# Kernel tuning notes

Hardware: AMD Instinct MI355X
Metric: run time of the kernel (lower is better)

Reference implementation:

```python
import math
import jax, jax.numpy as jnp
import numpy as np

B, T, C, H = 2, 1024, 1024, 16
D = C // H
NEG = -jnp.inf


def setup_inputs() -> dict:
    key = jax.random.key(0)
    ks = jax.random.split(key, 4)
    x_star = jax.random.normal(ks[0], (B, T, C), jnp.float32)
    x_hat = jax.random.normal(ks[1], (B, T, C), jnp.float32)
    # attn_masks semantics: True = keep. star-keys: causal; hat-keys: diagonal only.
    keep_star = jnp.broadcast_to(jnp.tril(jnp.ones((T, T), bool)), (B, T, T))
    keep_hat = jnp.broadcast_to(jnp.eye(T, dtype=bool), (B, T, T))
    W_attn = jax.random.normal(ks[2], (C, 3 * C), jnp.float32) * (1.0 / math.sqrt(C))
    b_attn = jnp.zeros((3 * C,), jnp.float32)
    W_proj = jax.random.normal(ks[3], (C, C), jnp.float32) * (1.0 / math.sqrt(C))
    b_proj = jnp.zeros((C,), jnp.float32)
    return dict(x_star=x_star, x_hat=x_hat, keep_star=keep_star, keep_hat=keep_hat,
                W_attn=W_attn, b_attn=b_attn, W_proj=W_proj, b_proj=b_proj)


def _interleave(x_star, x_hat, keep_star, keep_hat, W_attn, b_attn, W_proj, b_proj):
    def qkv(x):
        q, k, v = jnp.split(x @ W_attn + b_attn, 3, axis=-1)
        r = lambda t: t.reshape(B, T, H, D).transpose(0, 2, 1, 3)  # (B,H,T,D)
        return r(q), r(k), r(v)

    q_s, k_s, v_s = qkv(x_star)
    q_h, k_h, v_h = qkv(x_hat)

    scale = 1.0 / math.sqrt(D)
    attend = lambda q, k: jnp.einsum('bhqd,bhkd->bhqk', q, k) * scale

    # blocking masks (True = block), broadcast over heads
    mask_star = ~keep_star[:, None, :, :]
    mask_hat = ~keep_hat[:, None, :, :]
    mask_causal = ~jnp.tril(jnp.ones((T, T), bool))[None, None]

    def mlp(y):  # (B,H,T,D) -> (B,T,C)
        y = y.transpose(0, 2, 1, 3).reshape(B, T, C)
        return y @ W_proj + b_proj  # resid_dropout is identity in eval

    # star stream: plain causal self-attention
    att_star = jnp.where(mask_causal, NEG, attend(q_s, k_s))
    y_star = mlp(jax.nn.softmax(att_star, axis=-1) @ v_s)

    # hat stream: merge two score streams (hat queries vs star keys / hat keys)
    att_hs = jnp.where(mask_star, NEG, attend(q_h, k_s))
    att_hh = jnp.where(mask_hat, NEG, attend(q_h, k_h))
    merged = jnp.where(jnp.isinf(att_hh), att_hs, att_hh)
    p = jax.nn.softmax(merged, axis=-1)
    y_hat = (jnp.where(mask_star, 0.0, p) @ v_s
             + jnp.where(mask_hat, 0.0, p) @ v_h)
    y_hat = mlp(y_hat)
    return y_star, y_hat


def reference(x_star, x_hat, keep_star, keep_hat, W_attn, b_attn, W_proj, b_proj):
    return _interleave(x_star, x_hat, keep_star, keep_hat, W_attn, b_attn, W_proj, b_proj)
```

## Files before the change

kernel.cpp:

```cpp
#include <hip/hip_runtime.h>
#include <math.h>

#define T_ 1024
#define C_ 1024
#define H_ 16
#define D_ 64
#define B_ 2
#define M2 (B_*T_*C_)
#define QSC 0.18033688f

typedef __attribute__((ext_vector_type(8))) short bf16x8;
typedef __attribute__((ext_vector_type(8))) unsigned short ushort8;
typedef __attribute__((ext_vector_type(4))) float f32x4;

__device__ inline float fast_exp2(float x) {
  return __builtin_amdgcn_exp2f(x);
}

__device__ inline unsigned short f2bf(float f) {
  unsigned int u = __float_as_uint(f);
  u += 0x7fff + ((u >> 16) & 1);
  return (unsigned short)(u >> 16);
}
__device__ inline float bf2f(unsigned short u) {
  return __uint_as_float(((unsigned int)u) << 16);
}
__device__ inline unsigned int pack2bf(float lo, float hi) {
  unsigned int ul = __float_as_uint(lo);
  unsigned int uh = __float_as_uint(hi);
  ul += 0x7fff + ((ul >> 16) & 1);
  uh += 0x7fff + ((uh >> 16) & 1);
  return (ul >> 16) | (uh & 0xffff0000u);
}

__device__ inline void load16(unsigned short* lds, const unsigned short* g) {
  __builtin_amdgcn_global_load_lds(
      (const __attribute__((address_space(1))) unsigned int*)g,
      (__attribute__((address_space(3))) unsigned int*)lds, 16, 0, 0);
}

__device__ void transpose_tile(const float* __restrict__ Win,
                               unsigned short* __restrict__ Wout, int N,
                               int n0, int k0, float (*Ts)[65], int tid)
{
#pragma unroll
  for (int p = 0; p < 4; ++p) {
    int chunk = tid + p * 256;
    int r = chunk >> 4, c4 = chunk & 15;
    float4 v = *(const float4*)(Win + (size_t)(k0 + r) * N + n0 + c4 * 4);
    Ts[r][c4*4+0] = v.x; Ts[r][c4*4+1] = v.y;
    Ts[r][c4*4+2] = v.z; Ts[r][c4*4+3] = v.w;
  }
  __syncthreads();
#pragma unroll
  for (int p = 0; p < 2; ++p) {
    int chunk = tid + p * 256;
    int n = chunk >> 3, kq = chunk & 7;
    ushort8 o;
#pragma unroll
    for (int j = 0; j < 8; ++j) o[j] = f2bf(Ts[kq * 8 + j][n]);
    *(ushort8*)(Wout + (size_t)(n0 + n) * 1024 + k0 + kq * 8) = o;
  }
}

__global__ __launch_bounds__(256) void prepass(
    const float* __restrict__ xs, const float* __restrict__ xh,
    const float* __restrict__ Wa, const float* __restrict__ Wp,
    unsigned short* __restrict__ Xbf, unsigned short* __restrict__ WaT,
    unsigned short* __restrict__ WpT)
{
  __shared__ float Ts[64][65];
  const int bid = blockIdx.x;
  const int tid = threadIdx.x;
  if (bid < 4096) {
    size_t c = (size_t)bid * 256 + tid;
    size_t e = c * 4;
    const float* src = (e < (size_t)2048 * 1024) ? (xs + e)
                                                 : (xh + e - (size_t)2048 * 1024);
    float4 v = *(const float4*)src;
    ushort4 o;
    o.x = f2bf(v.x); o.y = f2bf(v.y); o.z = f2bf(v.z); o.w = f2bf(v.w);
    *(ushort4*)(Xbf + e) = o;
  } else if (bid < 4864) {
    int t = bid - 4096;
    transpose_tile(Wa, WaT, 3072, (t % 48) * 64, (t / 48) * 64, Ts, tid);
  } else {
    int t = bid - 4864;
    transpose_tile(Wp, WpT, 1024, (t % 16) * 64, (t / 16) * 64, Ts, tid);
  }
}

__global__ __launch_bounds__(512) void qkv_mfma(
    const unsigned short* __restrict__ A,
    const unsigned short* __restrict__ Bt,
    const float* __restrict__ bias,
    unsigned short* __restrict__ qkv)
{
  __shared__ __align__(16) unsigned short As[128 * 64];
  __shared__ __align__(16) unsigned short Bs[128 * 64];
  const int tid = threadIdx.x;
  const int col0 = blockIdx.x * 128;
  const int row0 = blockIdx.y * 128;
  const int w = tid >> 6, lane = tid & 63;
  const int lane16 = lane & 15, quad = lane >> 4;
  const int wm = w >> 2, wn = w & 3;
  f32x4 acc[4][2];
#pragma unroll
  for (int mt = 0; mt < 4; ++mt)
#pragma unroll
    for (int nt = 0; nt < 2; ++nt) acc[mt][nt] = (f32x4){0.f, 0.f, 0.f, 0.f};

  for (int k0 = 0; k0 < 1024; k0 += 64) {
    __syncthreads();
#pragma unroll
    for (int it = 0; it < 2; ++it) {
      int chunk = tid + it * 512;
      int row = chunk >> 3, cq = chunk & 7, gq = cq ^ (row & 7);
      load16(As + chunk * 8, A  + (size_t)(row0 + row) * 1024 + k0 + gq * 8);
      load16(Bs + chunk * 8, Bt + (size_t)(col0 + row) * 1024 + k0 + gq * 8);
    }
    __syncthreads();
#pragma unroll
    for (int kb = 0; kb < 2; ++kb) {
      bf16x8 af[4], bfr[2];
      int q = kb * 4 + quad;
#pragma unroll
      for (int mt = 0; mt < 4; ++mt) {
        int m = wm * 64 + mt * 16 + lane16;
        af[mt] = *(const bf16x8*)&As[m * 64 + (q ^ (m & 7)) * 8];
      }
#pragma unroll
      for (int nt = 0; nt < 2; ++nt) {
        int n = wn * 32 + nt * 16 + lane16;
        bfr[nt] = *(const bf16x8*)&Bs[n * 64 + (q ^ (n & 7)) * 8];
      }
#pragma unroll
      for (int mt = 0; mt < 4; ++mt)
#pragma unroll
        for (int nt = 0; nt < 2; ++nt)
          acc[mt][nt] = __builtin_amdgcn_mfma_f32_16x16x32_bf16(
              af[mt], bfr[nt], acc[mt][nt], 0, 0, 0);
    }
  }

#pragma unroll
  for (int mt = 0; mt < 4; ++mt) {
#pragma unroll
    for (int nt = 0; nt < 2; ++nt) {
      int gn = col0 + wn * 32 + nt * 16 + lane16;
      int which = gn >> 10, c = gn & 1023;
      int h = c >> 6, d = c & 63;
      float bv = bias[gn];
#pragma unroll
      for (int r = 0; r < 4; ++r) {
        int gm = row0 + wm * 64 + mt * 16 + quad * 4 + r;
        int s = gm >> 11, b = (gm >> 10) & 1, t = gm & 1023;
        float val = acc[mt][nt][r] + bv;
        if (which == 0) val *= QSC;
        size_t idx;
        if (which == 2 && s == 0)
          idx = (size_t)2 * M2 + ((size_t)(b * 16 + h) * 64 + d) * 1024 + t;
        else
          idx = (size_t)(s * 3 + which) * M2 +
                ((size_t)(b * 16 + h) * 1024 + t) * 64 + d;
        qkv[idx] = f2bf(val);
      }
    }
  }
}

__global__ __launch_bounds__(256) void proj_mfma(
    const unsigned short* __restrict__ A,
    const unsigned short* __restrict__ Bt,
    const float* __restrict__ bias,
    float* __restrict__ out)
{
  __shared__ __align__(16) unsigned short As[128 * 64];
  __shared__ __align__(16) unsigned short Bs[64 * 64];
  const int tid = threadIdx.x;
  const int col0 = blockIdx.x * 64;
  const int row0 = blockIdx.y * 128;
  const int w = tid >> 6, lane = tid & 63;
  const int lane16 = lane & 15, quad = lane >> 4;
  const int wm = w >> 1, wn = w & 1;
  f32x4 acc[4][2];
#pragma unroll
  for (int mt = 0; mt < 4; ++mt)
#pragma unroll
    for (int nt = 0; nt < 2; ++nt) acc[mt][nt] = (f32x4){0.f, 0.f, 0.f, 0.f};

  for (int k0 = 0; k0 < 1024; k0 += 64) {
    __syncthreads();
#pragma unroll
    for (int it = 0; it < 4; ++it) {
      int chunk = tid + it * 256;
      int row = chunk >> 3, cq = chunk & 7, gq = cq ^ (row & 7);
      load16(As + chunk * 8, A + (size_t)(row0 + row) * 1024 + k0 + gq * 8);
    }
#pragma unroll
    for (int it = 0; it < 2; ++it) {
      int chunk = tid + it * 256;
      int row = chunk >> 3, cq = chunk & 7, gq = cq ^ (row & 7);
      load16(Bs + chunk * 8, Bt + (size_t)(col0 + row) * 1024 + k0 + gq * 8);
    }
    __syncthreads();
#pragma unroll
    for (int kb = 0; kb < 2; ++kb) {
      bf16x8 af[4], bfr[2];
      int q = kb * 4 + quad;
#pragma unroll
      for (int mt = 0; mt < 4; ++mt) {
        int m = wm * 64 + mt * 16 + lane16;
        af[mt] = *(const bf16x8*)&As[m * 64 + (q ^ (m & 7)) * 8];
      }
#pragma unroll
      for (int nt = 0; nt < 2; ++nt) {
        int n = wn * 32 + nt * 16 + lane16;
        bfr[nt] = *(const bf16x8*)&Bs[n * 64 + (q ^ (n & 7)) * 8];
      }
#pragma unroll
      for (int mt = 0; mt < 4; ++mt)
#pragma unroll
        for (int nt = 0; nt < 2; ++nt)
          acc[mt][nt] = __builtin_amdgcn_mfma_f32_16x16x32_bf16(
              af[mt], bfr[nt], acc[mt][nt], 0, 0, 0);
    }
  }

#pragma unroll
  for (int mt = 0; mt < 4; ++mt) {
#pragma unroll
    for (int nt = 0; nt < 2; ++nt) {
      int gn = col0 + wn * 32 + nt * 16 + lane16;
      float bv = bias[gn];
#pragma unroll
      for (int r = 0; r < 4; ++r) {
        int gm = row0 + wm * 64 + mt * 16 + quad * 4 + r;
        out[(size_t)gm * 1024 + gn] = acc[mt][nt][r] + bv;
      }
    }
  }
}

__global__ __launch_bounds__(256) void attn_fused(
    const unsigned short* __restrict__ ws, unsigned short* __restrict__ Y)
{
  __shared__ __align__(16) unsigned short Qss[64 * 64];
  __shared__ __align__(16) unsigned short Qsh[64 * 64];
  __shared__ __align__(16) unsigned short Ks[2][64 * 64];
  __shared__ __align__(16) unsigned short Vts[2][64 * 64];
  __shared__ __align__(16) unsigned short Ps[4][2][16][72];
  __shared__ float diag[64];

  const int tid = threadIdx.x;
  const int bx  = blockIdx.x;
  const int inner = bx & 31;
  const int h = inner & 15;
  const int b = (inner >> 4) & 1;
  const int qt = 15 - (bx >> 5);
  const int i0 = qt * 64;
  const size_t hb = (size_t)(b * H_ + h) * T_ * D_;

  const unsigned short* Qsg = ws + (size_t)0 * M2 + hb;
  const unsigned short* Kg  = ws + (size_t)1 * M2 + hb;
  const unsigned short* VTg = ws + (size_t)2 * M2 + hb;
  const unsigned short* Qhg = ws + (size_t)3 * M2 + hb;
  const unsigned short* Khg = ws + (size_t)4 * M2 + hb;
  const unsigned short* Vhg = ws + (size_t)5 * M2 + hb;

  const int lane = tid & 63;
  const int w = tid >> 6;
  const int lane16 = lane & 15, quad = lane >> 4;
  const int wq0 = w * 16;

#pragma unroll
  for (int it = 0; it < 2; ++it) {
    int ch = tid + it * 256;
    int row = ch >> 3, cq = ch & 7, gq = cq ^ (row & 7);
    load16(Qss + ch * 8, Qsg + (size_t)(i0 + row) * 64 + gq * 8);
    load16(Qsh + ch * 8, Qhg + (size_t)(i0 + row) * 64 + gq * 8);
    load16(&Ks[0][ch * 8], Kg + (size_t)row * 64 + gq * 8);
    load16(&Vts[0][ch * 8], VTg + (size_t)row * 1024 + gq * 8);
  }
  __syncthreads();

  bf16x8 qf[2][2];
  {
    int m = wq0 + lane16;
    qf[0][0] = *(const bf16x8*)&Qss[m * 64 + ((quad) ^ (m & 7)) * 8];
    qf[0][1] = *(const bf16x8*)&Qss[m * 64 + ((4 + quad) ^ (m & 7)) * 8];
    qf[1][0] = *(const bf16x8*)&Qsh[m * 64 + ((quad) ^ (m & 7)) * 8];
    qf[1][1] = *(const bf16x8*)&Qsh[m * 64 + ((4 + quad) ^ (m & 7)) * 8];
  }
  if (tid < 64) {
    const unsigned short* kh = Khg + (size_t)(i0 + tid) * 64;
    float sum = 0.f;
#pragma unroll
    for (int c = 0; c < 8; ++c) {
      bf16x8 qv = *(const bf16x8*)&Qsh[tid * 64 + (c ^ (tid & 7)) * 8];
      ushort8 kv = *(const ushort8*)(kh + c * 8);
#pragma unroll
      for (int j = 0; j < 8; ++j)
        sum += bf2f((unsigned short)qv[j]) * bf2f(kv[j]);
    }
    diag[tid] = sum;
  }
  __syncthreads();

  float lacc[2] = {0.f, 0.f};
  f32x4 O[2][4];
#pragma unroll
  for (int st = 0; st < 2; ++st)
#pragma unroll
    for (int nt = 0; nt < 4; ++nt) O[st][nt] = (f32x4){0.f, 0.f, 0.f, 0.f};
  const int kstar = wq0 + lane16;

  for (int kt = 0; kt <= qt; ++kt) {
    const int cur = kt & 1;
    if (kt < qt) {
      const int nxt = 1 - cur;
#pragma unroll
      for (int it = 0; it < 2; ++it) {
        int ch = tid + it * 256;
        int row = ch >> 3, cq = ch & 7, gq = cq ^ (row & 7);
        load16(&Ks[nxt][ch * 8], Kg + (size_t)((kt + 1) * 64 + row) * 64 + gq * 8);
        load16(&Vts[nxt][ch * 8], VTg + (size_t)row * 1024 + (kt + 1) * 64 + gq * 8);
      }
    }

    bf16x8 kf[2][4], vf[2][4];
#pragma unroll
    for (int kb = 0; kb < 2; ++kb) {
      int q = kb * 4 + quad;
#pragma unroll
      for (int mt = 0; mt < 4; ++mt) {
        int m = mt * 16 + lane16;
        kf[kb][mt] = *(const bf16x8*)&Ks[cur][m * 64 + (q ^ (m & 7)) * 8];
        vf[kb][mt] = *(const bf16x8*)&Vts[cur][m * 64 + (q ^ (m & 7)) * 8];
      }
    }

    f32x4 St[2][4];
#pragma unroll
    for (int st = 0; st < 2; ++st)
#pragma unroll
      for (int mt = 0; mt < 4; ++mt) St[st][mt] = (f32x4){0.f, 0.f, 0.f, 0.f};
#pragma unroll
    for (int kb = 0; kb < 2; ++kb)
#pragma unroll
      for (int st = 0; st < 2; ++st)
#pragma unroll
        for (int mt = 0; mt < 4; ++mt)
          St[st][mt] = __builtin_amdgcn_mfma_f32_16x16x32_bf16(
              kf[kb][mt], qf[st][kb], St[st][mt], 0, 0, 0);

    if (kt == qt) {
      const float dv = diag[kstar];
#pragma unroll
      for (int mt = 0; mt < 4; ++mt)
#pragma unroll
        for (int r = 0; r < 4; ++r) {
          int key = mt * 16 + quad * 4 + r;
          if (key > kstar) { St[0][mt][r] = -INFINITY; St[1][mt][r] = -INFINITY; }
          if (key == kstar) St[1][mt][r] = dv;
        }
    }

#pragma unroll
    for (int st = 0; st < 2; ++st) {
      float rsum = 0.f;
#pragma unroll
      for (int mt = 0; mt < 4; ++mt)
#pragma unroll
        for (int r = 0; r < 4; ++r) {
          float p = fast_exp2(St[st][mt][r]);
          St[st][mt][r] = p;
          rsum += p;
        }
      lacc[st] += rsum;
    }

#pragma unroll
    for (int st = 0; st < 2; ++st)
#pragma unroll
      for (int mt = 0; mt < 4; ++mt) {
        *(unsigned int*)&Ps[w][st][lane16][mt * 16 + quad * 4] =
            pack2bf(St[st][mt][0], St[st][mt][1]);
        *(unsigned int*)&Ps[w][st][lane16][mt * 16 + quad * 4 + 2] =
            pack2bf(St[st][mt][2], St[st][mt][3]);
      }

#pragma unroll
    for (int kb = 0; kb < 2; ++kb) {
      bf16x8 pa[2];
#pragma unroll
      for (int st = 0; st < 2; ++st)
        pa[st] = *(const bf16x8*)&Ps[w][st][lane16][kb * 32 + quad * 8];
#pragma unroll
      for (int st = 0; st < 2; ++st)
#pragma unroll
        for (int nt = 0; nt < 4; ++nt)
          O[st][nt] = __builtin_amdgcn_mfma_f32_16x16x32_bf16(
              pa[st], vf[kb][nt], O[st][nt], 0, 0, 0);
    }

    if (kt == qt) {
      float pd = fast_exp2(diag[kstar]);
      float p4[4];
#pragma unroll
      for (int r = 0; r < 4; ++r) p4[r] = __shfl(pd, quad * 4 + r, 16);
#pragma unroll
      for (int r = 0; r < 4; ++r) {
        const unsigned short* vh = Vhg + (size_t)(i0 + wq0 + quad * 4 + r) * 64;
#pragma unroll
        for (int nt = 0; nt < 4; ++nt)
          O[1][nt][r] += p4[r] * bf2f(vh[nt * 16 + lane16]);
      }
    }
    __syncthreads();
  }

#pragma unroll
  for (int st = 0; st < 2; ++st) {
    lacc[st] += __shfl_xor(lacc[st], 16, 64);
    lacc[st] += __shfl_xor(lacc[st], 32, 64);
  }
  float l4[2][4];
#pragma unroll
  for (int st = 0; st < 2; ++st)
#pragma unroll
    for (int r = 0; r < 4; ++r)
      l4[st][r] = __shfl(lacc[st], quad * 4 + r, 16);
#pragma unroll
  for (int r = 0; r < 4; ++r) {
    int gi = i0 + wq0 + quad * 4 + r;
    float invs = 1.f / l4[0][r];
    float invh = 1.f / l4[1][r];
    unsigned short* ys = Y + ((size_t)(b * 1024 + gi)) * 1024 + h * 64;
    unsigned short* yh = Y + ((size_t)(2048 + b * 1024 + gi)) * 1024 + h * 64;
#pragma unroll
    for (int nt = 0; nt < 4; ++nt) {
      ys[nt * 16 + lane16] = f2bf(O[0][nt][r] * invs);
      yh[nt * 16 + lane16] = f2bf(O[1][nt][r] * invh);
    }
  }
}

extern "C" void kernel_launch(void* const* d_in, const int* in_sizes, int n_in,
                              void* d_out, int out_size, void* d_ws, size_t ws_size,
                              hipStream_t stream) {
  (void)in_sizes; (void)n_in; (void)out_size; (void)ws_size;
  const float* xs = (const float*)d_in[0];
  const float* xh = (const float*)d_in[1];
  const float* Wa = (const float*)d_in[4];
  const float* ba = (const float*)d_in[5];
  const float* Wp = (const float*)d_in[6];
  const float* bp = (const float*)d_in[7];

  unsigned short* qkv = (unsigned short*)d_ws;
  unsigned short* Ybf = qkv + (size_t)6 * M2;
  unsigned short* Xbf = Ybf + (size_t)4 * 1024 * 1024;
  unsigned short* WaT = Xbf + (size_t)4 * 1024 * 1024;
  unsigned short* WpT = WaT + (size_t)3 * 1024 * 1024;
  float* out = (float*)d_out;

  prepass   <<<5120, 256, 0, stream>>>(xs, xh, Wa, Wp, Xbf, WaT, WpT);
  qkv_mfma  <<<dim3(24, 32), 512, 0, stream>>>(Xbf, WaT, ba, qkv);
  attn_fused<<<dim3(512), 256, 0, stream>>>(qkv, Ybf);
  proj_mfma <<<dim3(16, 32), 256, 0, stream>>>(Ybf, WpT, bp, out);
}
```

Measured before the change: 181.5 us.

## Fuse all four stages into one persistent cooperative kernel with grid syncs

Replaces the four separate launches (prepass, QKV GEMM, attention, projection) with a single cooperative kernel of 512 blocks that runs each stage in turn, separated by grid-wide barriers. The QKV GEMM is retiled to 128x192 tiles so that 512 blocks cover it, and the attention and projection stages reuse the shared-memory buffer. The aim is to remove kernel launch gaps and tail effects between stages. In exchange, each stage is limited to 512 blocks at two blocks per CU, grid.sync adds its own cost, and the larger QKV tile may raise register pressure. If the cooperative launch fails, the code falls back to the original four kernels.

```diff
diff --git a/kernel.cpp b/kernel.cpp
--- a/kernel.cpp
+++ b/kernel.cpp
@@ -1,5 +1,8 @@
 #include <hip/hip_runtime.h>
+#include <hip/hip_cooperative_groups.h>
 #include <math.h>
+
+namespace cg = cooperative_groups;
 
 #define T_ 1024
 #define C_ 1024
@@ -8,6 +11,7 @@
 #define B_ 2
 #define M2 (B_*T_*C_)
 #define QSC 0.18033688f
+#define LDSZ 51456
 
 typedef __attribute__((ext_vector_type(8))) short bf16x8;
 typedef __attribute__((ext_vector_type(8))) unsigned short ushort8;
@@ -16,7 +20,6 @@
 __device__ inline float fast_exp2(float x) {
   return __builtin_amdgcn_exp2f(x);
 }
-
 __device__ inline unsigned short f2bf(float f) {
   unsigned int u = __float_as_uint(f);
   u += 0x7fff + ((u >> 16) & 1);
@@ -32,16 +35,15 @@
   uh += 0x7fff + ((uh >> 16) & 1);
   return (ul >> 16) | (uh & 0xffff0000u);
 }
-
 __device__ inline void load16(unsigned short* lds, const unsigned short* g) {
   __builtin_amdgcn_global_load_lds(
       (const __attribute__((address_space(1))) unsigned int*)g,
       (__attribute__((address_space(3))) unsigned int*)lds, 16, 0, 0);
 }
 
-__device__ void transpose_tile(const float* __restrict__ Win,
-                               unsigned short* __restrict__ Wout, int N,
-                               int n0, int k0, float (*Ts)[65], int tid)
+__device__ inline void transpose_tile(const float* __restrict__ Win,
+                                      unsigned short* __restrict__ Wout, int N,
+                                      int n0, int k0, float (*Ts)[65], int tid)
 {
 #pragma unroll
   for (int p = 0; p < 4; ++p) {
@@ -60,6 +62,393 @@
 #pragma unroll
     for (int j = 0; j < 8; ++j) o[j] = f2bf(Ts[kq * 8 + j][n]);
     *(ushort8*)(Wout + (size_t)(n0 + n) * 1024 + k0 + kq * 8) = o;
+  }
+  __syncthreads();
+}
+
+__global__ __launch_bounds__(256, 2) void mega(
+    const float* __restrict__ xs, const float* __restrict__ xh,
+    const float* __restrict__ Wa, const float* __restrict__ ba,
+    const float* __restrict__ Wp, const float* __restrict__ bp,
+    unsigned short* __restrict__ qkv, unsigned short* __restrict__ Ybf,
+    unsigned short* __restrict__ Xbf, unsigned short* __restrict__ WaT,
+    unsigned short* __restrict__ WpT, float* __restrict__ out)
+{
+  extern __shared__ __align__(16) char smem[];
+  cg::grid_group grid = cg::this_grid();
+  const int tid = threadIdx.x;
+  const int bx  = blockIdx.x;
+
+  {
+    float (*Ts)[65] = (float (*)[65])smem;
+#pragma unroll 1
+    for (int u = bx; u < 5120; u += 512) {
+      if (u < 4096) {
+        size_t c = (size_t)u * 256 + tid;
+        size_t e = c * 4;
+        const float* src = (e < (size_t)2048 * 1024)
+                               ? (xs + e) : (xh + e - (size_t)2048 * 1024);
+        float4 v = *(const float4*)src;
+        ushort4 o;
+        o.x = f2bf(v.x); o.y = f2bf(v.y); o.z = f2bf(v.z); o.w = f2bf(v.w);
+        *(ushort4*)(Xbf + e) = o;
+      } else if (u < 4864) {
+        int t = u - 4096;
+        transpose_tile(Wa, WaT, 3072, (t % 48) * 64, (t / 48) * 64, Ts, tid);
+      } else {
+        int t = u - 4864;
+        transpose_tile(Wp, WpT, 1024, (t % 16) * 64, (t / 16) * 64, Ts, tid);
+      }
+    }
+  }
+  grid.sync();
+
+  {
+    unsigned short* As = (unsigned short*)smem;
+    unsigned short* Bs = (unsigned short*)(smem + 16384);
+    const int w = tid >> 6, lane = tid & 63;
+    const int lane16 = lane & 15, quad = lane >> 4;
+    const int wm = w >> 1, wn = w & 1;
+    const int col0 = (bx & 15) * 192;
+    const int row0 = (bx >> 4) * 128;
+    f32x4 acc[4][6];
+#pragma unroll
+    for (int mt = 0; mt < 4; ++mt)
+#pragma unroll
+      for (int nt = 0; nt < 6; ++nt) acc[mt][nt] = (f32x4){0.f, 0.f, 0.f, 0.f};
+
+    for (int k0 = 0; k0 < 1024; k0 += 64) {
+      __syncthreads();
+#pragma unroll
+      for (int it = 0; it < 4; ++it) {
+        int ch = tid + it * 256;
+        int row = ch >> 3, cq = ch & 7, gq = cq ^ (row & 7);
+        load16(As + ch * 8, Xbf + (size_t)(row0 + row) * 1024 + k0 + gq * 8);
+      }
+#pragma unroll
+      for (int it = 0; it < 6; ++it) {
+        int ch = tid + it * 256;
+        int row = ch >> 3, cq = ch & 7, gq = cq ^ (row & 7);
+        load16(Bs + ch * 8, WaT + (size_t)(col0 + row) * 1024 + k0 + gq * 8);
+      }
+      __syncthreads();
+#pragma unroll
+      for (int kb = 0; kb < 2; ++kb) {
+        bf16x8 af[4], bfr[6];
+        int q = kb * 4 + quad;
+#pragma unroll
+        for (int mt = 0; mt < 4; ++mt) {
+          int m = wm * 64 + mt * 16 + lane16;
+          af[mt] = *(const bf16x8*)&As[m * 64 + (q ^ (m & 7)) * 8];
+        }
+#pragma unroll
+        for (int nt = 0; nt < 6; ++nt) {
+          int n = wn * 96 + nt * 16 + lane16;
+          bfr[nt] = *(const bf16x8*)&Bs[n * 64 + (q ^ (n & 7)) * 8];
+        }
+#pragma unroll
+        for (int mt = 0; mt < 4; ++mt)
+#pragma unroll
+          for (int nt = 0; nt < 6; ++nt)
+            acc[mt][nt] = __builtin_amdgcn_mfma_f32_16x16x32_bf16(
+                af[mt], bfr[nt], acc[mt][nt], 0, 0, 0);
+      }
+    }
+#pragma unroll
+    for (int mt = 0; mt < 4; ++mt) {
+#pragma unroll
+      for (int nt = 0; nt < 6; ++nt) {
+        int gn = col0 + wn * 96 + nt * 16 + lane16;
+        int which = gn >> 10, c2 = gn & 1023;
+        int hh = c2 >> 6, dd = c2 & 63;
+        float bv = ba[gn];
+#pragma unroll
+        for (int r = 0; r < 4; ++r) {
+          int gm = row0 + wm * 64 + mt * 16 + quad * 4 + r;
+          int ss = gm >> 11, bb = (gm >> 10) & 1, t = gm & 1023;
+          float val = acc[mt][nt][r] + bv;
+          if (which == 0) val *= QSC;
+          size_t idx;
+          if (which == 2 && ss == 0)
+            idx = (size_t)2 * M2 + ((size_t)(bb * 16 + hh) * 64 + dd) * 1024 + t;
+          else
+            idx = (size_t)(ss * 3 + which) * M2 +
+                  ((size_t)(bb * 16 + hh) * 1024 + t) * 64 + dd;
+          qkv[idx] = f2bf(val);
+        }
+      }
+    }
+  }
+  grid.sync();
+
+  {
+    unsigned short* Ks0 = (unsigned short*)smem;
+    unsigned short* Ks1 = (unsigned short*)(smem + 8192);
+    unsigned short* Vt0 = (unsigned short*)(smem + 16384);
+    unsigned short* Vt1 = (unsigned short*)(smem + 24576);
+    unsigned short* PsB = (unsigned short*)(smem + 32768);
+    float* diag = (float*)(smem + 51200);
+
+    const int inner = bx & 31;
+    const int h = inner & 15;
+    const int b = (inner >> 4) & 1;
+    const int g = bx >> 5;
+    const int qt = (bx < 256) ? (15 - g) : (g - 8);
+    const int i0 = qt * 64;
+    const size_t hb = (size_t)(b * H_ + h) * T_ * D_;
+
+    const unsigned short* Qsg = qkv + (size_t)0 * M2 + hb;
+    const unsigned short* Kg  = qkv + (size_t)1 * M2 + hb;
+    const unsigned short* VTg = qkv + (size_t)2 * M2 + hb;
+    const unsigned short* Qhg = qkv + (size_t)3 * M2 + hb;
+    const unsigned short* Khg = qkv + (size_t)4 * M2 + hb;
+    const unsigned short* Vhg = qkv + (size_t)5 * M2 + hb;
+
+    const int lane = tid & 63;
+    const int w = tid >> 6;
+    const int lane16 = lane & 15, quad = lane >> 4;
+    const int wq0 = w * 16;
+
+    bf16x8 qf[2][2];
+    {
+      const unsigned short* qs = Qsg + (size_t)(i0 + wq0 + lane16) * 64;
+      const unsigned short* qh = Qhg + (size_t)(i0 + wq0 + lane16) * 64;
+      qf[0][0] = *(const bf16x8*)(qs + quad * 8);
+      qf[0][1] = *(const bf16x8*)(qs + 32 + quad * 8);
+      qf[1][0] = *(const bf16x8*)(qh + quad * 8);
+      qf[1][1] = *(const bf16x8*)(qh + 32 + quad * 8);
+    }
+    if (tid < 64) {
+      const unsigned short* qh = Qhg + (size_t)(i0 + tid) * 64;
+      const unsigned short* kh = Khg + (size_t)(i0 + tid) * 64;
+      float sum = 0.f;
+#pragma unroll
+      for (int c2 = 0; c2 < 8; ++c2) {
+        ushort8 qv = *(const ushort8*)(qh + c2 * 8);
+        ushort8 kv = *(const ushort8*)(kh + c2 * 8);
+#pragma unroll
+        for (int j = 0; j < 8; ++j) sum += bf2f(qv[j]) * bf2f(kv[j]);
+      }
+      diag[tid] = sum;
+    }
+#pragma unroll
+    for (int it = 0; it < 2; ++it) {
+      int ch = tid + it * 256;
+      int row = ch >> 3, cq = ch & 7, gq = cq ^ (row & 7);
+      load16(Ks0 + ch * 8, Kg + (size_t)row * 64 + gq * 8);
+      load16(Vt0 + ch * 8, VTg + (size_t)row * 1024 + gq * 8);
+    }
+    __syncthreads();
+
+    float lacc[2] = {0.f, 0.f};
+    f32x4 O[2][4];
+#pragma unroll
+    for (int st = 0; st < 2; ++st)
+#pragma unroll
+      for (int nt = 0; nt < 4; ++nt) O[st][nt] = (f32x4){0.f, 0.f, 0.f, 0.f};
+    const int kstar = wq0 + lane16;
+
+    for (int kt = 0; kt <= qt; ++kt) {
+      unsigned short* KsCur = (kt & 1) ? Ks1 : Ks0;
+      unsigned short* VtCur = (kt & 1) ? Vt1 : Vt0;
+      if (kt < qt) {
+        unsigned short* KsNxt = (kt & 1) ? Ks0 : Ks1;
+        unsigned short* VtNxt = (kt & 1) ? Vt0 : Vt1;
+#pragma unroll
+        for (int it = 0; it < 2; ++it) {
+          int ch = tid + it * 256;
+          int row = ch >> 3, cq = ch & 7, gq = cq ^ (row & 7);
+          load16(KsNxt + ch * 8, Kg + (size_t)((kt + 1) * 64 + row) * 64 + gq * 8);
+          load16(VtNxt + ch * 8, VTg + (size_t)row * 1024 + (kt + 1) * 64 + gq * 8);
+        }
+      }
+
+      bf16x8 kf[2][4], vf[2][4];
+#pragma unroll
+      for (int kb = 0; kb < 2; ++kb) {
+        int q = kb * 4 + quad;
+#pragma unroll
+        for (int mt = 0; mt < 4; ++mt) {
+          int m = mt * 16 + lane16;
+          kf[kb][mt] = *(const bf16x8*)&KsCur[m * 64 + (q ^ (m & 7)) * 8];
+          vf[kb][mt] = *(const bf16x8*)&VtCur[m * 64 + (q ^ (m & 7)) * 8];
+        }
+      }
+
+      f32x4 St[2][4];
+#pragma unroll
+      for (int st = 0; st < 2; ++st)
+#pragma unroll
+        for (int mt = 0; mt < 4; ++mt) St[st][mt] = (f32x4){0.f, 0.f, 0.f, 0.f};
+#pragma unroll
+      for (int kb = 0; kb < 2; ++kb)
+#pragma unroll
+        for (int st = 0; st < 2; ++st)
+#pragma unroll
+          for (int mt = 0; mt < 4; ++mt)
+            St[st][mt] = __builtin_amdgcn_mfma_f32_16x16x32_bf16(
+                kf[kb][mt], qf[st][kb], St[st][mt], 0, 0, 0);
+
+      if (kt == qt) {
+        const float dv = diag[kstar];
+#pragma unroll
+        for (int mt = 0; mt < 4; ++mt)
+#pragma unroll
+          for (int r = 0; r < 4; ++r) {
+            int key = mt * 16 + quad * 4 + r;
+            if (key > kstar) { St[0][mt][r] = -INFINITY; St[1][mt][r] = -INFINITY; }
+            if (key == kstar) St[1][mt][r] = dv;
+          }
+      }
+
+#pragma unroll
+      for (int st = 0; st < 2; ++st) {
+        float rsum = 0.f;
+#pragma unroll
+        for (int mt = 0; mt < 4; ++mt)
+#pragma unroll
+          for (int r = 0; r < 4; ++r) {
+            float p = fast_exp2(St[st][mt][r]);
+            St[st][mt][r] = p;
+            rsum += p;
+          }
+        lacc[st] += rsum;
+      }
+
+#pragma unroll
+      for (int st = 0; st < 2; ++st) {
+        unsigned short* prow = PsB + (size_t)((w * 2 + st) * 16 + lane16) * 72;
+#pragma unroll
+        for (int mt = 0; mt < 4; ++mt) {
+          *(unsigned int*)&prow[mt * 16 + quad * 4] =
+              pack2bf(St[st][mt][0], St[st][mt][1]);
+          *(unsigned int*)&prow[mt * 16 + quad * 4 + 2] =
+              pack2bf(St[st][mt][2], St[st][mt][3]);
+        }
+      }
+
+#pragma unroll
+      for (int kb = 0; kb < 2; ++kb) {
+        bf16x8 pa[2];
+#pragma unroll
+        for (int st = 0; st < 2; ++st)
+          pa[st] = *(const bf16x8*)&PsB[(size_t)((w * 2 + st) * 16 + lane16) * 72 +
+                                        kb * 32 + quad * 8];
+#pragma unroll
+        for (int st = 0; st < 2; ++st)
+#pragma unroll
+          for (int nt = 0; nt < 4; ++nt)
+            O[st][nt] = __builtin_amdgcn_mfma_f32_16x16x32_bf16(
+                pa[st], vf[kb][nt], O[st][nt], 0, 0, 0);
+      }
+
+      if (kt == qt) {
+        float pd = fast_exp2(diag[kstar]);
+        float p4[4];
+#pragma unroll
+        for (int r = 0; r < 4; ++r) p4[r] = __shfl(pd, quad * 4 + r, 16);
+#pragma unroll
+        for (int r = 0; r < 4; ++r) {
+          const unsigned short* vh = Vhg + (size_t)(i0 + wq0 + quad * 4 + r) * 64;
+#pragma unroll
+          for (int nt = 0; nt < 4; ++nt)
+            O[1][nt][r] += p4[r] * bf2f(vh[nt * 16 + lane16]);
+        }
+      }
+      __syncthreads();
+    }
+
+#pragma unroll
+    for (int st = 0; st < 2; ++st) {
+      lacc[st] += __shfl_xor(lacc[st], 16, 64);
+      lacc[st] += __shfl_xor(lacc[st], 32, 64);
+    }
+    float l4[2][4];
+#pragma unroll
+    for (int st = 0; st < 2; ++st)
+#pragma unroll
+      for (int r = 0; r < 4; ++r)
+        l4[st][r] = __shfl(lacc[st], quad * 4 + r, 16);
+#pragma unroll
+    for (int r = 0; r < 4; ++r) {
+      int gi = i0 + wq0 + quad * 4 + r;
+      float invs = 1.f / l4[0][r];
+      float invh = 1.f / l4[1][r];
+      unsigned short* ys = Ybf + ((size_t)(b * 1024 + gi)) * 1024 + h * 64;
+      unsigned short* yh = Ybf + ((size_t)(2048 + b * 1024 + gi)) * 1024 + h * 64;
+#pragma unroll
+      for (int nt = 0; nt < 4; ++nt) {
+        ys[nt * 16 + lane16] = f2bf(O[0][nt][r] * invs);
+        yh[nt * 16 + lane16] = f2bf(O[1][nt][r] * invh);
+      }
+    }
+  }
+  grid.sync();
+
+  {
+    unsigned short* As = (unsigned short*)smem;
+    unsigned short* Bs = (unsigned short*)(smem + 16384);
+    const int w = tid >> 6, lane = tid & 63;
+    const int lane16 = lane & 15, quad = lane >> 4;
+    const int wm = w >> 1, wn = w & 1;
+    const int col0 = (bx & 15) * 64;
+    const int row0 = (bx >> 4) * 128;
+    f32x4 acc[4][2];
+#pragma unroll
+    for (int mt = 0; mt < 4; ++mt)
+#pragma unroll
+      for (int nt = 0; nt < 2; ++nt) acc[mt][nt] = (f32x4){0.f, 0.f, 0.f, 0.f};
+
+    for (int k0 = 0; k0 < 1024; k0 += 64) {
+      __syncthreads();
+#pragma unroll
+      for (int it = 0; it < 4; ++it) {
+        int ch = tid + it * 256;
+        int row = ch >> 3, cq = ch & 7, gq = cq ^ (row & 7);
+        load16(As + ch * 8, Ybf + (size_t)(row0 + row) * 1024 + k0 + gq * 8);
+      }
+#pragma unroll
+      for (int it = 0; it < 2; ++it) {
+        int ch = tid + it * 256;
+        int row = ch >> 3, cq = ch & 7, gq = cq ^ (row & 7);
+        load16(Bs + ch * 8, WpT + (size_t)(col0 + row) * 1024 + k0 + gq * 8);
+      }
+      __syncthreads();
+#pragma unroll
+      for (int kb = 0; kb < 2; ++kb) {
+        bf16x8 af[4], bfr[2];
+        int q = kb * 4 + quad;
+#pragma unroll
+        for (int mt = 0; mt < 4; ++mt) {
+          int m = wm * 64 + mt * 16 + lane16;
+          af[mt] = *(const bf16x8*)&As[m * 64 + (q ^ (m & 7)) * 8];
+        }
+#pragma unroll
+        for (int nt = 0; nt < 2; ++nt) {
+          int n = wn * 32 + nt * 16 + lane16;
+          bfr[nt] = *(const bf16x8*)&Bs[n * 64 + (q ^ (n & 7)) * 8];
+        }
+#pragma unroll
+        for (int mt = 0; mt < 4; ++mt)
+#pragma unroll
+          for (int nt = 0; nt < 2; ++nt)
+            acc[mt][nt] = __builtin_amdgcn_mfma_f32_16x16x32_bf16(
+                af[mt], bfr[nt], acc[mt][nt], 0, 0, 0);
+      }
+    }
+#pragma unroll
+    for (int mt = 0; mt < 4; ++mt) {
+#pragma unroll
+      for (int nt = 0; nt < 2; ++nt) {
+        int gn = col0 + wn * 32 + nt * 16 + lane16;
+        float bv = bp[gn];
+#pragma unroll
+        for (int r = 0; r < 4; ++r) {
+          int gm = row0 + wm * 64 + mt * 16 + quad * 4 + r;
+          out[(size_t)gm * 1024 + gn] = acc[mt][nt][r] + bv;
+        }
+      }
+    }
   }
 }
 
@@ -91,10 +480,8 @@
 }
 
 __global__ __launch_bounds__(512) void qkv_mfma(
-    const unsigned short* __restrict__ A,
-    const unsigned short* __restrict__ Bt,
-    const float* __restrict__ bias,
-    unsigned short* __restrict__ qkv)
+    const unsigned short* __restrict__ A, const unsigned short* __restrict__ Bt,
+    const float* __restrict__ bias, unsigned short* __restrict__ qkv)
 {
   __shared__ __align__(16) unsigned short As[128 * 64];
   __shared__ __align__(16) unsigned short Bs[128 * 64];
@@ -109,7 +496,6 @@
   for (int mt = 0; mt < 4; ++mt)
 #pragma unroll
     for (int nt = 0; nt < 2; ++nt) acc[mt][nt] = (f32x4){0.f, 0.f, 0.f, 0.f};
-
   for (int k0 = 0; k0 < 1024; k0 += 64) {
     __syncthreads();
 #pragma unroll
@@ -142,7 +528,6 @@
               af[mt], bfr[nt], acc[mt][nt], 0, 0, 0);
     }
   }
-
 #pragma unroll
   for (int mt = 0; mt < 4; ++mt) {
 #pragma unroll
@@ -170,10 +555,8 @@
 }
 
 __global__ __launch_bounds__(256) void proj_mfma(
-    const unsigned short* __restrict__ A,
-    const unsigned short* __restrict__ Bt,
-    const float* __restrict__ bias,
-    float* __restrict__ out)
+    const unsigned short* __restrict__ A, const unsigned short* __restrict__ Bt,
+    const float* __restrict__ bias, float* __restrict__ out)
 {
   __shared__ __align__(16) unsigned short As[128 * 64];
   __shared__ __align__(16) unsigned short Bs[64 * 64];
@@ -188,7 +571,6 @@
   for (int mt = 0; mt < 4; ++mt)
 #pragma unroll
     for (int nt = 0; nt < 2; ++nt) acc[mt][nt] = (f32x4){0.f, 0.f, 0.f, 0.f};
-
   for (int k0 = 0; k0 < 1024; k0 += 64) {
     __syncthreads();
 #pragma unroll
@@ -226,7 +608,6 @@
               af[mt], bfr[nt], acc[mt][nt], 0, 0, 0);
     }
   }
-
 #pragma unroll
   for (int mt = 0; mt < 4; ++mt) {
 #pragma unroll
@@ -327,7 +708,6 @@
         load16(&Vts[nxt][ch * 8], VTg + (size_t)row * 1024 + (kt + 1) * 64 + gq * 8);
       }
     }
-
     bf16x8 kf[2][4], vf[2][4];
 #pragma unroll
     for (int kb = 0; kb < 2; ++kb) {
@@ -339,7 +719,6 @@
         vf[kb][mt] = *(const bf16x8*)&Vts[cur][m * 64 + (q ^ (m & 7)) * 8];
       }
     }
-
     f32x4 St[2][4];
 #pragma unroll
     for (int st = 0; st < 2; ++st)
@@ -353,7 +732,6 @@
         for (int mt = 0; mt < 4; ++mt)
           St[st][mt] = __builtin_amdgcn_mfma_f32_16x16x32_bf16(
               kf[kb][mt], qf[st][kb], St[st][mt], 0, 0, 0);
-
     if (kt == qt) {
       const float dv = diag[kstar];
 #pragma unroll
@@ -365,7 +743,6 @@
           if (key == kstar) St[1][mt][r] = dv;
         }
     }
-
 #pragma unroll
     for (int st = 0; st < 2; ++st) {
       float rsum = 0.f;
@@ -379,7 +756,6 @@
         }
       lacc[st] += rsum;
     }
-
 #pragma unroll
     for (int st = 0; st < 2; ++st)
 #pragma unroll
@@ -389,7 +765,6 @@
         *(unsigned int*)&Ps[w][st][lane16][mt * 16 + quad * 4 + 2] =
             pack2bf(St[st][mt][2], St[st][mt][3]);
       }
-
 #pragma unroll
     for (int kb = 0; kb < 2; ++kb) {
       bf16x8 pa[2];
@@ -403,7 +778,6 @@
           O[st][nt] = __builtin_amdgcn_mfma_f32_16x16x32_bf16(
               pa[st], vf[kb][nt], O[st][nt], 0, 0, 0);
     }
-
     if (kt == qt) {
       float pd = fast_exp2(diag[kstar]);
       float p4[4];
@@ -419,7 +793,6 @@
     }
     __syncthreads();
   }
-
 #pragma unroll
   for (int st = 0; st < 2; ++st) {
     lacc[st] += __shfl_xor(lacc[st], 16, 64);
@@ -464,8 +837,16 @@
   unsigned short* WpT = WaT + (size_t)3 * 1024 * 1024;
   float* out = (float*)d_out;
 
-  prepass   <<<5120, 256, 0, stream>>>(xs, xh, Wa, Wp, Xbf, WaT, WpT);
-  qkv_mfma  <<<dim3(24, 32), 512, 0, stream>>>(Xbf, WaT, ba, qkv);
-  attn_fused<<<dim3(512), 256, 0, stream>>>(qkv, Ybf);
-  proj_mfma <<<dim3(16, 32), 256, 0, stream>>>(Ybf, WpT, bp, out);
-}
+  void* kargs[] = {(void*)&xs, (void*)&xh, (void*)&Wa, (void*)&ba,
+                   (void*)&Wp, (void*)&bp, (void*)&qkv, (void*)&Ybf,
+                   (void*)&Xbf, (void*)&WaT, (void*)&WpT, (void*)&out};
+  hipError_t err = hipLaunchCooperativeKernel(
+      (const void*)mega, dim3(512), dim3(256), kargs, (unsigned int)LDSZ, stream);
+  if (err != hipSuccess) {
+    (void)hipGetLastError();
+    prepass   <<<5120, 256, 0, stream>>>(xs, xh, Wa, Wp, Xbf, WaT, WpT);
+    qkv_mfma  <<<dim3(24, 32), 512, 0, stream>>>(Xbf, WaT, ba, qkv);
+    attn_fused<<<dim3(512), 256, 0, stream>>>(qkv, Ybf);
+    proj_mfma <<<dim3(16, 32), 256, 0, stream>>>(Ybf, WpT, bp, out);
+  }
+}
```

New measurement: 388.0 us. +113.8%, slower.
